# Optimization experiments

Measured on AMD Instinct MI355X. Metric: run time of the kernel, lower is better.

## Reference

```python
import jax, jax.numpy as jnp
import numpy as np

B, S, I, H = 16, 4096, 256, 256
H_CYCLES, L_CYCLES = 2, 3


def setup_inputs() -> dict:
    key = jax.random.key(0)
    ks = jax.random.split(key, 18)
    g = lambda k, shape, s=0.05: jax.random.normal(k, shape, dtype=jnp.float32) * s
    return {
        "x": g(ks[0], (B, S, I), 1.0),
        "h0": jnp.zeros((1, B, H), jnp.float32),
        # GRU (PyTorch layout: rows ordered [reset, update, new])
        "gru_w_ih": g(ks[1], (3 * H, I)),
        "gru_w_hh": g(ks[2], (3 * H, H)),
        "gru_b_ih": g(ks[3], (3 * H,)),
        "gru_b_hh": g(ks[4], (3 * H,)),
        # L refine cell
        "Lg_w": g(ks[5], (H, 2 * H)), "Lg_b": g(ks[6], (H,)),
        "Lt_w": g(ks[7], (H, 2 * H)), "Lt_b": g(ks[8], (H,)),
        "Lu_w": g(ks[9], (H, H)),     "Lu_b": g(ks[10], (H,)),
        # H refine cell
        "Hg_w": g(ks[11], (H, 2 * H)), "Hg_b": g(ks[12], (H,)),
        "Ht_w": g(ks[13], (H, 2 * H)), "Ht_b": g(ks[14], (H,)),
        "Hu_w": g(ks[15], (H, H)),     "Hu_b": g(ks[16], (H,)),
    }


def _refine_cell(prev, hid, gw, gb, tw, tb, uw, ub):
    c = jnp.concatenate([prev, hid], axis=-1)            # (B, 2H)
    gate = jax.nn.sigmoid(c @ gw.T + gb)
    refinement = jnp.tanh(c @ tw.T + tb)
    out = gate * refinement + (1.0 - gate) * prev
    new_hid = jnp.tanh(out @ uw.T + ub)
    return out, new_hid


def reference(x, h0, gru_w_ih, gru_w_hh, gru_b_ih, gru_b_hh,
              Lg_w, Lg_b, Lt_w, Lt_b, Lu_w, Lu_b,
              Hg_w, Hg_b, Ht_w, Ht_b, Hu_w, Hu_b):
    # ---- GRU (single layer, batch_first), PyTorch gate equations ----
    x_proj = x @ gru_w_ih.T + gru_b_ih                   # (B, S, 3H)

    def gru_step(h, xp):
        hp = h @ gru_w_hh.T + gru_b_hh                   # (B, 3H)
        xr, xz, xn = jnp.split(xp, 3, axis=-1)
        hr, hz, hn = jnp.split(hp, 3, axis=-1)
        r = jax.nn.sigmoid(xr + hr)
        z = jax.nn.sigmoid(xz + hz)
        n = jnp.tanh(xn + r * hn)
        h_new = (1.0 - z) * n + z * h
        return h_new, h_new

    h_last, base_out = jax.lax.scan(gru_step, h0[0], x_proj.transpose(1, 0, 2))
    # base_out: (S, B, H)

    # ---- hierarchical recursive refinement; zH/zL persist across t ----
    def refine_step(carry, out_t):
        zH, zL = carry
        o = out_t
        for _ in range(H_CYCLES):
            for _ in range(L_CYCLES):
                o, zL = _refine_cell(o, zH, Lg_w, Lg_b, Lt_w, Lt_b, Lu_w, Lu_b)
            o, zH = _refine_cell(o, zL, Hg_w, Hg_b, Ht_w, Ht_b, Hu_w, Hu_b)
        return (zH, zL), o

    z0 = jnp.zeros((x.shape[0], H), x.dtype)
    _, refined = jax.lax.scan(refine_step, (z0, z0), base_out)  # (S, B, H)
    output = refined.transpose(1, 0, 2)                  # (B, S, H)
    return output, h_last[None]                          # hidden: (1, B, H)
```

## Files before the change

### kernel.cpp

```cpp
#include <hip/hip_runtime.h>
#include <math.h>


#define NB   16
#define SEQ  4096
#define TEAMS 8
#define WPT  32
#define BPT  2
#define NTH  256

typedef unsigned long long u64;

__device__ __forceinline__ float fexp(float v){ return __builtin_amdgcn_exp2f(v*1.44269504089f); }
__device__ __forceinline__ float sigf(float v){ return __builtin_amdgcn_rcpf(1.f + fexp(-v)); }
__device__ __forceinline__ float ftanh(float v){ return 2.f*sigf(2.f*v) - 1.f; }

__device__ __forceinline__ void swpw(u64* p, u64 v){
  (void)__hip_atomic_exchange(p, v, __ATOMIC_RELAXED, __HIP_MEMORY_SCOPE_AGENT);
}
__device__ __forceinline__ u64 ldw(const u64* p){
  return __hip_atomic_load(p, __ATOMIC_RELAXED, __HIP_MEMORY_SCOPE_AGENT);
}

typedef _Float16 h2f __attribute__((ext_vector_type(2)));
typedef __fp16   h2p __attribute__((ext_vector_type(2)));
union H2U { h2f f; h2p p; unsigned u; };
__device__ __forceinline__ unsigned pk2(float lo, float hi){
  H2U t; t.p = __builtin_amdgcn_cvt_pkrtz(lo, hi); return t.u;
}
__device__ __forceinline__ float2 upk2(unsigned w){
  H2U t; t.u = w; float2 r; r.x = (float)t.f.x; r.y = (float)t.f.y; return r;
}
__device__ __forceinline__ u64 packh(float lo, float hi, unsigned tag){
  return ((u64)tag<<32) | (u64)pk2(lo, hi);
}

#define WGBAR() asm volatile("s_waitcnt lgkmcnt(0)\n\ts_barrier" ::: "memory")

extern "C" __global__ __launch_bounds__(NTH, 1)
void trm_kernel(const float* __restrict__ x,   const float* __restrict__ h0,
                const float* __restrict__ wih, const float* __restrict__ whh,
                const float* __restrict__ bih, const float* __restrict__ bhh,
                const float* __restrict__ Lgw, const float* __restrict__ Lgb,
                const float* __restrict__ Ltw, const float* __restrict__ Ltb,
                const float* __restrict__ Luw, const float* __restrict__ Lub,
                const float* __restrict__ Hgw, const float* __restrict__ Hgb,
                const float* __restrict__ Htw, const float* __restrict__ Htb,
                const float* __restrict__ Huw, const float* __restrict__ Hub,
                float* __restrict__ out, u64* __restrict__ act_base)
{
  const int team = blockIdx.x & (TEAMS-1);
  const int j    = blockIdx.x / TEAMS;
  const int tid  = threadIdx.x;

  __shared__ float wgRZ[16][520];
  __shared__ float wgX[8][264];
  __shared__ float wgN[8][264];
  __shared__ float wclG[8][520], wclT[8][520];
  __shared__ float wchG[8][520], wchT[8][520];
  __shared__ float wul[8][264],  wuh[8][264];
  __shared__ float xst [BPT][256];
  __shared__ float st_o [BPT][256];
  __shared__ float st_zh[BPT][256];
  __shared__ float st_zl[BPT][256];
  __shared__ float st_h [BPT][256];
  __shared__ float exvA[16][2], exvB[16][2];
  __shared__ float bR[8],bZ[8],bX[8],bN[8],bCLg[8],bCLt[8],bCHg[8],bCHt[8],bUL[8],bUH[8];

  {
    const int k = tid;
    for (int r=0;r<8;r++){
      const int nr = j*8+r;
      wgRZ[r][k]       = wih[(size_t)nr*256+k];
      wgRZ[r][256+k]   = whh[(size_t)nr*256+k];
      wgRZ[8+r][k]     = wih[(size_t)(256+nr)*256+k];
      wgRZ[8+r][256+k] = whh[(size_t)(256+nr)*256+k];
      wgX[r][k] = wih[(size_t)(512+nr)*256+k];
      wgN[r][k] = whh[(size_t)(512+nr)*256+k];
      wclG[r][k] = Lgw[(size_t)nr*512+k];  wclG[r][256+k] = Lgw[(size_t)nr*512+256+k];
      wclT[r][k] = Ltw[(size_t)nr*512+k];  wclT[r][256+k] = Ltw[(size_t)nr*512+256+k];
      wchG[r][k] = Hgw[(size_t)nr*512+k];  wchG[r][256+k] = Hgw[(size_t)nr*512+256+k];
      wchT[r][k] = Htw[(size_t)nr*512+k];  wchT[r][256+k] = Htw[(size_t)nr*512+256+k];
      wul[r][k] = Luw[(size_t)nr*256+k];
      wuh[r][k] = Huw[(size_t)nr*256+k];
    }
    if (tid<8){
      const int nr = j*8+tid;
      bR[tid]  = bih[nr]     + bhh[nr];
      bZ[tid]  = bih[256+nr] + bhh[256+nr];
      bX[tid]  = bih[512+nr];
      bN[tid]  = bhh[512+nr];
      bCLg[tid]= Lgb[nr];  bCLt[tid]= Ltb[nr];
      bCHg[tid]= Hgb[nr];  bCHt[tid]= Htb[nr];
      bUL[tid] = Lub[nr];  bUH[tid] = Hub[nr];
    }
    for (int u=tid; u<BPT*256; u+=NTH){
      const int b=u>>8, i=u&255;
      st_h[b][i]  = h0[(team*BPT+b)*256+i];
      st_o[b][i]  = 0.f;
      st_zh[b][i] = 0.f;
      st_zl[b][i] = 0.f;
    }
  }
  __syncthreads();

  u64* actT = act_base + (size_t)team*4096;
  unsigned kst = 0;
  const bool wr0 = (j == 0);

  auto cstage = [&](float (*WG)[520], float (*WT)[520], float* bG, float* bT,
                    float (*hid)[256], bool wout, int tt){
    const unsigned tag = kst + 1u;
    u64* buf = actT + (kst & 1u)*1024;
    WGBAR();
    const int u = tid>>4, kk = tid&15, r = u&7;
    const bool isT = (u>=8);
    const float* wr = isT? WT[r] : WG[r];
    float a0=0.f, a1=0.f;
    #pragma unroll
    for (int i=0;i<16;i++){
      const float w = wr[kk+16*i];
      a0 += w*st_o[0][kk+16*i];
      a1 += w*st_o[1][kk+16*i];
    }
    #pragma unroll
    for (int i=0;i<16;i++){
      const float w = wr[256+kk+16*i];
      a0 += w*hid[0][kk+16*i];
      a1 += w*hid[1][kk+16*i];
    }
    a0 += __shfl_xor(a0,1); a0 += __shfl_xor(a0,2); a0 += __shfl_xor(a0,4); a0 += __shfl_xor(a0,8);
    a1 += __shfl_xor(a1,1); a1 += __shfl_xor(a1,2); a1 += __shfl_xor(a1,4); a1 += __shfl_xor(a1,8);
    if (kk==0){ exvA[u][0] = a0; exvA[u][1] = a1; }
    WGBAR();
    if (tid < 16){
      const int b = tid&1, rr = tid>>1;
      const float g = sigf (exvA[rr][b]   + bG[rr]);
      const float T = ftanh(exvA[8+rr][b] + bT[rr]);
      swpw(&buf[b*256 + j*8 + rr], packh(g, T, tag));
    }
    u64 w0, w1;
    for(;;){
      w0 = ldw(&buf[tid]); w1 = ldw(&buf[256+tid]);
      if ((unsigned)(w0>>32) >= tag && (unsigned)(w1>>32) >= tag) break;
      __builtin_amdgcn_s_sleep(1);
    }
    const float2 gt0 = upk2((unsigned)w0);
    const float2 gt1 = upk2((unsigned)w1);
    const float o0 = gt0.x*gt0.y + (1.f-gt0.x)*st_o[0][tid];
    const float o1 = gt1.x*gt1.y + (1.f-gt1.x)*st_o[1][tid];
    st_o[0][tid] = o0;
    st_o[1][tid] = o1;
    if (wout && wr0){
      out[((size_t)(team*BPT+0)*SEQ + tt)*256 + tid] = o0;
      out[((size_t)(team*BPT+1)*SEQ + tt)*256 + tid] = o1;
    }
    kst++;
  };

  auto ustage = [&](float (*W)[264], float* bU, float (*dst)[256]){
    const unsigned tag = kst + 1u;
    u64* buf = actT + (kst & 1u)*1024;
    WGBAR();
    const int u = tid>>5, kk = tid&31;
    const float* wr = W[u];
    float a0=0.f, a1=0.f;
    #pragma unroll
    for (int i=0;i<8;i++){
      const float w = wr[kk+32*i];
      a0 += w*st_o[0][kk+32*i];
      a1 += w*st_o[1][kk+32*i];
    }
    a0 += __shfl_xor(a0,1); a0 += __shfl_xor(a0,2); a0 += __shfl_xor(a0,4); a0 += __shfl_xor(a0,8); a0 += __shfl_xor(a0,16);
    a1 += __shfl_xor(a1,1); a1 += __shfl_xor(a1,2); a1 += __shfl_xor(a1,4); a1 += __shfl_xor(a1,8); a1 += __shfl_xor(a1,16);
    if (kk==0){ exvA[u][0] = a0; exvA[u][1] = a1; }
    WGBAR();
    if (tid < 8){
      const float v0 = ftanh(exvA[tid][0] + bU[tid]);
      const float v1 = ftanh(exvA[tid][1] + bU[tid]);
      swpw(&buf[j*8 + tid], packh(v0, v1, tag));
    }
    u64 w0;
    for(;;){
      w0 = ldw(&buf[tid]);
      if ((unsigned)(w0>>32) >= tag) break;
      __builtin_amdgcn_s_sleep(1);
    }
    const float2 v = upk2((unsigned)w0);
    dst[0][tid] = v.x;
    dst[1][tid] = v.y;
    kst++;
  };

  float px0 = x[((size_t)(team*BPT+0)*SEQ + 0)*256 + tid];
  float px1 = x[((size_t)(team*BPT+1)*SEQ + 0)*256 + tid];

  #pragma unroll 1
  for (int t=0; t<SEQ; ++t){
    {
      const unsigned tag = kst + 1u;
      u64* buf = actT + (kst & 1u)*1024;
      WGBAR();
      xst[0][tid] = px0;
      xst[1][tid] = px1;
      WGBAR();
      const int u = tid>>4, kk = tid&15, r = u&7;
      {
        const float* wr = wgRZ[u];
        float a0=0.f, a1=0.f;
        #pragma unroll
        for (int i=0;i<16;i++){
          const float w = wr[kk+16*i];
          a0 += w*xst[0][kk+16*i];
          a1 += w*xst[1][kk+16*i];
        }
        #pragma unroll
        for (int i=0;i<16;i++){
          const float w = wr[256+kk+16*i];
          a0 += w*st_h[0][kk+16*i];
          a1 += w*st_h[1][kk+16*i];
        }
        a0 += __shfl_xor(a0,1); a0 += __shfl_xor(a0,2); a0 += __shfl_xor(a0,4); a0 += __shfl_xor(a0,8);
        a1 += __shfl_xor(a1,1); a1 += __shfl_xor(a1,2); a1 += __shfl_xor(a1,4); a1 += __shfl_xor(a1,8);
        if (kk==0){ exvA[u][0] = a0; exvA[u][1] = a1; }
      }
      {
        const bool isH = (u>=8);
        const float* wr = isH? wgN[r] : wgX[r];
        float (*src)[256] = isH? st_h : xst;
        float a0=0.f, a1=0.f;
        #pragma unroll
        for (int i=0;i<16;i++){
          const float w = wr[kk+16*i];
          a0 += w*src[0][kk+16*i];
          a1 += w*src[1][kk+16*i];
        }
        a0 += __shfl_xor(a0,1); a0 += __shfl_xor(a0,2); a0 += __shfl_xor(a0,4); a0 += __shfl_xor(a0,8);
        a1 += __shfl_xor(a1,1); a1 += __shfl_xor(a1,2); a1 += __shfl_xor(a1,4); a1 += __shfl_xor(a1,8);
        if (kk==0){ exvB[u][0] = a0; exvB[u][1] = a1; }
      }
      WGBAR();
      if (tid < 16){
        const int b = tid&1, rr = tid>>1;
        const float pr = exvA[rr][b]   + bR[rr];
        const float pz = exvA[8+rr][b] + bZ[rr];
        const float xn = exvB[rr][b]   + bX[rr];
        const float hn = exvB[8+rr][b] + bN[rr];
        const float rg = sigf(pr);
        const float zg = sigf(pz);
        const float ng = ftanh(xn + rg*hn);
        swpw(&buf[b*256 + j*8 + rr], packh(ng, zg, tag));
      }
      u64 w0, w1;
      for(;;){
        w0 = ldw(&buf[tid]); w1 = ldw(&buf[256+tid]);
        if ((unsigned)(w0>>32) >= tag && (unsigned)(w1>>32) >= tag) break;
        __builtin_amdgcn_s_sleep(1);
      }
      const float2 nz0 = upk2((unsigned)w0);
      const float2 nz1 = upk2((unsigned)w1);
      const float h0v = (1.f-nz0.y)*nz0.x + nz0.y*st_h[0][tid];
      const float h1v = (1.f-nz1.y)*nz1.x + nz1.y*st_h[1][tid];
      st_h[0][tid] = h0v;  st_o[0][tid] = h0v;
      st_h[1][tid] = h1v;  st_o[1][tid] = h1v;
      if (t == SEQ-1 && wr0){
        out[(size_t)NB*SEQ*256 + (team*BPT+0)*256 + tid] = h0v;
        out[(size_t)NB*SEQ*256 + (team*BPT+1)*256 + tid] = h1v;
      }
      if (t+1 < SEQ){
        px0 = x[((size_t)(team*BPT+0)*SEQ + (t+1))*256 + tid];
        px1 = x[((size_t)(team*BPT+1)*SEQ + (t+1))*256 + tid];
      }
      kst++;
    }
    #pragma unroll 1
    for (int c=0;c<2;c++){
      cstage(wclG,wclT,bCLg,bCLt,st_zh,false,t);
      cstage(wclG,wclT,bCLg,bCLt,st_zh,false,t);
      cstage(wclG,wclT,bCLg,bCLt,st_zh,false,t);
      ustage(wul,bUL,st_zl);
      cstage(wchG,wchT,bCHg,bCHt,st_zl,(c==1),t);
      ustage(wuh,bUH,st_zh);
    }
  }
}

extern "C" void kernel_launch(void* const* d_in, const int* in_sizes, int n_in,
                              void* d_out, int out_size, void* d_ws, size_t ws_size,
                              hipStream_t stream)
{
  (void)hipMemsetAsync(d_ws, 0, (size_t)TEAMS*4096*sizeof(u64), stream);
  u64* act = (u64*)d_ws;

  dim3 grid(TEAMS*WPT), block(NTH);
  hipLaunchKernelGGL(trm_kernel, grid, block, 0, stream,
    (const float*)d_in[0],  (const float*)d_in[1],
    (const float*)d_in[2],  (const float*)d_in[3],
    (const float*)d_in[4],  (const float*)d_in[5],
    (const float*)d_in[6],  (const float*)d_in[7],
    (const float*)d_in[8],  (const float*)d_in[9],
    (const float*)d_in[10], (const float*)d_in[11],
    (const float*)d_in[12], (const float*)d_in[13],
    (const float*)d_in[14], (const float*)d_in[15],
    (const float*)d_in[16], (const float*)d_in[17],
    (float*)d_out, act);
}
```

Before: 97.89 ms.

## Overlap next GRU step with refinement stages and use single wide poll loads

Moves the GRU gate computation for step t+1 into the first refine stage of step t. It writes to a separate double-buffered global exchange area, so the GRU exchange latency is hidden behind the refine chain and each timestep no longer has a dedicated GRU cross-block barrier. The exchange buffers are interleaved by batch so each thread polls both values with one 128-bit load. That load uses a cache-bypassing inline-asm instruction, and x is now prefetched two steps ahead. The cost is more complex cross-stage dependencies, plus extra work and shared-memory state in the first refine stage.

```diff
diff --git a/kernel.cpp b/kernel.cpp
--- a/kernel.cpp
+++ b/kernel.cpp
@@ -10,6 +10,7 @@
 #define NTH  256
 
 typedef unsigned long long u64;
+typedef unsigned u32x4 __attribute__((ext_vector_type(4)));
 
 __device__ __forceinline__ float fexp(float v){ return __builtin_amdgcn_exp2f(v*1.44269504089f); }
 __device__ __forceinline__ float sigf(float v){ return __builtin_amdgcn_rcpf(1.f + fexp(-v)); }
@@ -33,6 +34,18 @@
 }
 __device__ __forceinline__ u64 packh(float lo, float hi, unsigned tag){
   return ((u64)tag<<32) | (u64)pk2(lo, hi);
+}
+
+__device__ __forceinline__ void poll2x(const u64* p, unsigned tag,
+                                       unsigned &lo0, unsigned &lo1){
+  u32x4 v;
+  for(;;){
+    asm volatile("global_load_dwordx4 %0, %1, off sc0 sc1\n\ts_waitcnt vmcnt(0)"
+                 : "=&v"(v) : "v"(p) : "memory");
+    if (v.y >= tag && v.w >= tag) break;
+    __builtin_amdgcn_s_sleep(1);
+  }
+  lo0 = v.x; lo1 = v.z;
 }
 
 #define WGBAR() asm volatile("s_waitcnt lgkmcnt(0)\n\ts_barrier" ::: "memory")
@@ -64,7 +77,7 @@
   __shared__ float st_zh[BPT][256];
   __shared__ float st_zl[BPT][256];
   __shared__ float st_h [BPT][256];
-  __shared__ float exvA[16][2], exvB[16][2];
+  __shared__ float exvA[16][2], exvC[16][2], exvD[16][2];
   __shared__ float bR[8],bZ[8],bX[8],bN[8],bCLg[8],bCLt[8],bCHg[8],bCHt[8],bUL[8],bUH[8];
 
   {
@@ -94,22 +107,75 @@
       bCHg[tid]= Hgb[nr];  bCHt[tid]= Htb[nr];
       bUL[tid] = Lub[nr];  bUH[tid] = Hub[nr];
     }
-    for (int u=tid; u<BPT*256; u+=NTH){
-      const int b=u>>8, i=u&255;
-      st_h[b][i]  = h0[(team*BPT+b)*256+i];
-      st_o[b][i]  = 0.f;
-      st_zh[b][i] = 0.f;
-      st_zl[b][i] = 0.f;
-    }
+    st_h[0][tid]  = h0[(team*BPT+0)*256+tid];
+    st_h[1][tid]  = h0[(team*BPT+1)*256+tid];
+    st_o[0][tid]  = 0.f;  st_o[1][tid]  = 0.f;
+    st_zh[0][tid] = 0.f;  st_zh[1][tid] = 0.f;
+    st_zl[0][tid] = 0.f;  st_zl[1][tid] = 0.f;
+    xst[0][tid] = x[((size_t)(team*BPT+0)*SEQ + 0)*256 + tid];
+    xst[1][tid] = x[((size_t)(team*BPT+1)*SEQ + 0)*256 + tid];
   }
   __syncthreads();
 
   u64* actT = act_base + (size_t)team*4096;
+  u64* gb   = actT + 2048;
   unsigned kst = 0;
   const bool wr0 = (j == 0);
 
+  auto gru_produce = [&](int step){
+    const unsigned gt = (unsigned)step + 1u;
+    u64* g = gb + (size_t)(step & 1)*512;
+    const int u = tid>>4, kk = tid&15, r = u&7;
+    {
+      const float* wr = wgRZ[u];
+      float a0=0.f, a1=0.f;
+      #pragma unroll
+      for (int i=0;i<16;i++){
+        const float w = wr[kk+16*i];
+        a0 += w*xst[0][kk+16*i];
+        a1 += w*xst[1][kk+16*i];
+      }
+      #pragma unroll
+      for (int i=0;i<16;i++){
+        const float w = wr[256+kk+16*i];
+        a0 += w*st_h[0][kk+16*i];
+        a1 += w*st_h[1][kk+16*i];
+      }
+      a0 += __shfl_xor(a0,1); a0 += __shfl_xor(a0,2); a0 += __shfl_xor(a0,4); a0 += __shfl_xor(a0,8);
+      a1 += __shfl_xor(a1,1); a1 += __shfl_xor(a1,2); a1 += __shfl_xor(a1,4); a1 += __shfl_xor(a1,8);
+      if (kk==0){ exvC[u][0] = a0; exvC[u][1] = a1; }
+    }
+    {
+      const bool isH = (u>=8);
+      const float* wr = isH? wgN[r] : wgX[r];
+      float (*src)[256] = isH? st_h : xst;
+      float a0=0.f, a1=0.f;
+      #pragma unroll
+      for (int i=0;i<16;i++){
+        const float w = wr[kk+16*i];
+        a0 += w*src[0][kk+16*i];
+        a1 += w*src[1][kk+16*i];
+      }
+      a0 += __shfl_xor(a0,1); a0 += __shfl_xor(a0,2); a0 += __shfl_xor(a0,4); a0 += __shfl_xor(a0,8);
+      a1 += __shfl_xor(a1,1); a1 += __shfl_xor(a1,2); a1 += __shfl_xor(a1,4); a1 += __shfl_xor(a1,8);
+      if (kk==0){ exvD[u][0] = a0; exvD[u][1] = a1; }
+    }
+    WGBAR();
+    if (tid < 16){
+      const int b = tid&1, rr = tid>>1;
+      const float pr = exvC[rr][b]   + bR[rr];
+      const float pz = exvC[8+rr][b] + bZ[rr];
+      const float xn = exvD[rr][b]   + bX[rr];
+      const float hn = exvD[8+rr][b] + bN[rr];
+      const float rg = sigf(pr);
+      const float zg = sigf(pz);
+      const float ng = ftanh(xn + rg*hn);
+      swpw(&g[(size_t)(j*8+rr)*2 + b], packh(ng, zg, gt));
+    }
+  };
+
   auto cstage = [&](float (*WG)[520], float (*WT)[520], float* bG, float* bT,
-                    float (*hid)[256], bool wout, int tt){
+                    float (*hid)[256], bool wout, bool pg, int tt){
     const unsigned tag = kst + 1u;
     u64* buf = actT + (kst & 1u)*1024;
     WGBAR();
@@ -137,16 +203,13 @@
       const int b = tid&1, rr = tid>>1;
       const float g = sigf (exvA[rr][b]   + bG[rr]);
       const float T = ftanh(exvA[8+rr][b] + bT[rr]);
-      swpw(&buf[b*256 + j*8 + rr], packh(g, T, tag));
-    }
-    u64 w0, w1;
-    for(;;){
-      w0 = ldw(&buf[tid]); w1 = ldw(&buf[256+tid]);
-      if ((unsigned)(w0>>32) >= tag && (unsigned)(w1>>32) >= tag) break;
-      __builtin_amdgcn_s_sleep(1);
-    }
-    const float2 gt0 = upk2((unsigned)w0);
-    const float2 gt1 = upk2((unsigned)w1);
+      swpw(&buf[(size_t)(j*8+rr)*2 + b], packh(g, T, tag));
+    }
+    if (pg) gru_produce(tt+1);
+    unsigned lo0, lo1;
+    poll2x(&buf[2*tid], tag, lo0, lo1);
+    const float2 gt0 = upk2(lo0);
+    const float2 gt1 = upk2(lo1);
     const float o0 = gt0.x*gt0.y + (1.f-gt0.x)*st_o[0][tid];
     const float o1 = gt1.x*gt1.y + (1.f-gt1.x)*st_o[1][tid];
     st_o[0][tid] = o0;
@@ -192,94 +255,41 @@
     kst++;
   };
 
-  float px0 = x[((size_t)(team*BPT+0)*SEQ + 0)*256 + tid];
-  float px1 = x[((size_t)(team*BPT+1)*SEQ + 0)*256 + tid];
+  float px0 = x[((size_t)(team*BPT+0)*SEQ + 1)*256 + tid];
+  float px1 = x[((size_t)(team*BPT+1)*SEQ + 1)*256 + tid];
+  gru_produce(0);
 
   #pragma unroll 1
   for (int t=0; t<SEQ; ++t){
     {
-      const unsigned tag = kst + 1u;
-      u64* buf = actT + (kst & 1u)*1024;
       WGBAR();
-      xst[0][tid] = px0;
-      xst[1][tid] = px1;
-      WGBAR();
-      const int u = tid>>4, kk = tid&15, r = u&7;
-      {
-        const float* wr = wgRZ[u];
-        float a0=0.f, a1=0.f;
-        #pragma unroll
-        for (int i=0;i<16;i++){
-          const float w = wr[kk+16*i];
-          a0 += w*xst[0][kk+16*i];
-          a1 += w*xst[1][kk+16*i];
-        }
-        #pragma unroll
-        for (int i=0;i<16;i++){
-          const float w = wr[256+kk+16*i];
-          a0 += w*st_h[0][kk+16*i];
-          a1 += w*st_h[1][kk+16*i];
-        }
-        a0 += __shfl_xor(a0,1); a0 += __shfl_xor(a0,2); a0 += __shfl_xor(a0,4); a0 += __shfl_xor(a0,8);
-        a1 += __shfl_xor(a1,1); a1 += __shfl_xor(a1,2); a1 += __shfl_xor(a1,4); a1 += __shfl_xor(a1,8);
-        if (kk==0){ exvA[u][0] = a0; exvA[u][1] = a1; }
-      }
-      {
-        const bool isH = (u>=8);
-        const float* wr = isH? wgN[r] : wgX[r];
-        float (*src)[256] = isH? st_h : xst;
-        float a0=0.f, a1=0.f;
-        #pragma unroll
-        for (int i=0;i<16;i++){
-          const float w = wr[kk+16*i];
-          a0 += w*src[0][kk+16*i];
-          a1 += w*src[1][kk+16*i];
-        }
-        a0 += __shfl_xor(a0,1); a0 += __shfl_xor(a0,2); a0 += __shfl_xor(a0,4); a0 += __shfl_xor(a0,8);
-        a1 += __shfl_xor(a1,1); a1 += __shfl_xor(a1,2); a1 += __shfl_xor(a1,4); a1 += __shfl_xor(a1,8);
-        if (kk==0){ exvB[u][0] = a0; exvB[u][1] = a1; }
-      }
-      WGBAR();
-      if (tid < 16){
-        const int b = tid&1, rr = tid>>1;
-        const float pr = exvA[rr][b]   + bR[rr];
-        const float pz = exvA[8+rr][b] + bZ[rr];
-        const float xn = exvB[rr][b]   + bX[rr];
-        const float hn = exvB[8+rr][b] + bN[rr];
-        const float rg = sigf(pr);
-        const float zg = sigf(pz);
-        const float ng = ftanh(xn + rg*hn);
-        swpw(&buf[b*256 + j*8 + rr], packh(ng, zg, tag));
-      }
-      u64 w0, w1;
-      for(;;){
-        w0 = ldw(&buf[tid]); w1 = ldw(&buf[256+tid]);
-        if ((unsigned)(w0>>32) >= tag && (unsigned)(w1>>32) >= tag) break;
-        __builtin_amdgcn_s_sleep(1);
-      }
-      const float2 nz0 = upk2((unsigned)w0);
-      const float2 nz1 = upk2((unsigned)w1);
+      u64* g = gb + (size_t)(t & 1)*512;
+      unsigned lo0, lo1;
+      poll2x(&g[2*tid], (unsigned)(t+1), lo0, lo1);
+      const float2 nz0 = upk2(lo0);
+      const float2 nz1 = upk2(lo1);
       const float h0v = (1.f-nz0.y)*nz0.x + nz0.y*st_h[0][tid];
       const float h1v = (1.f-nz1.y)*nz1.x + nz1.y*st_h[1][tid];
       st_h[0][tid] = h0v;  st_o[0][tid] = h0v;
       st_h[1][tid] = h1v;  st_o[1][tid] = h1v;
+      xst[0][tid] = px0;
+      xst[1][tid] = px1;
+      if (t+2 < SEQ){
+        px0 = x[((size_t)(team*BPT+0)*SEQ + (t+2))*256 + tid];
+        px1 = x[((size_t)(team*BPT+1)*SEQ + (t+2))*256 + tid];
+      }
       if (t == SEQ-1 && wr0){
         out[(size_t)NB*SEQ*256 + (team*BPT+0)*256 + tid] = h0v;
         out[(size_t)NB*SEQ*256 + (team*BPT+1)*256 + tid] = h1v;
       }
-      if (t+1 < SEQ){
-        px0 = x[((size_t)(team*BPT+0)*SEQ + (t+1))*256 + tid];
-        px1 = x[((size_t)(team*BPT+1)*SEQ + (t+1))*256 + tid];
-      }
-      kst++;
     }
     #pragma unroll 1
     for (int c=0;c<2;c++){
-      cstage(wclG,wclT,bCLg,bCLt,st_zh,false,t);
-      cstage(wclG,wclT,bCLg,bCLt,st_zh,false,t);
-      cstage(wclG,wclT,bCLg,bCLt,st_zh,false,t);
+      cstage(wclG,wclT,bCLg,bCLt,st_zh,false,(c==0)&&(t+1<SEQ),t);
+      cstage(wclG,wclT,bCLg,bCLt,st_zh,false,false,t);
+      cstage(wclG,wclT,bCLg,bCLt,st_zh,false,false,t);
       ustage(wul,bUL,st_zl);
-      cstage(wchG,wchT,bCHg,bCHt,st_zl,(c==1),t);
+      cstage(wchG,wchT,bCHg,bCHt,st_zl,(c==1),false,t);
       ustage(wuh,bUH,st_zh);
     }
   }
```

After: 87.04 ms. 11.1% less time.
